# Performance work log

Measured on AMD Instinct MI355X. Metric: run time of the kernel, lower is better.

Reference implementation:

```python
import jax, jax.numpy as jnp
import numpy as np

B, S, D, H = 4, 2048, 512, 8
E = D // H  # d_head = 64

def setup_inputs() -> dict:
    key = jax.random.key(0)
    ks = jax.random.split(key, 10)
    s_in = (1.0 / np.sqrt(D))
    x  = jax.random.normal(ks[0], (B, S, D), dtype=jnp.float32)
    Wq = jax.random.normal(ks[1], (H, D, E), dtype=jnp.float32) * s_in
    bq = jax.random.normal(ks[2], (H, E), dtype=jnp.float32) * 0.01
    Wk = jax.random.normal(ks[3], (H, D, E), dtype=jnp.float32) * s_in
    bk = jax.random.normal(ks[4], (H, E), dtype=jnp.float32) * 0.01
    Wv = jax.random.normal(ks[5], (H, D, E), dtype=jnp.float32) * s_in
    bv = jax.random.normal(ks[6], (H, E), dtype=jnp.float32) * 0.01
    Wo = jax.random.normal(ks[7], (D, D), dtype=jnp.float32) * s_in
    bo = jax.random.normal(ks[8], (D,), dtype=jnp.float32) * 0.01
    return {"x": x, "Wq": Wq, "bq": bq, "Wk": Wk, "bk": bk,
            "Wv": Wv, "bv": bv, "Wo": Wo, "bo": bo}

def reference(x, Wq, bq, Wk, bk, Wv, bv, Wo, bo):
    B_, S_, D_ = x.shape
    # per-head projections (batched over head axis h)
    q = jnp.einsum('bsd,hde->bhse', x, Wq) + bq[None, :, None, :]
    k = jnp.einsum('bsd,hde->bhse', x, Wk) + bk[None, :, None, :]
    v = jnp.einsum('bsd,hde->bhse', x, Wv) + bv[None, :, None, :]
    # NOTE: original scales by d_model**-0.5 (full D), not d_head**-0.5
    scale = jnp.asarray(D_, x.dtype) ** -0.5
    scores = jnp.einsum('bhse,bhte->bhst', q, k) * scale  # [B,H,S,S]
    causal = jnp.tril(jnp.ones((S_, S_), dtype=bool))
    scores = jnp.where(causal[None, None], scores, -jnp.inf)
    attn = jax.nn.softmax(scores, axis=-1)
    out = jnp.einsum('bhst,bhte->bhse', attn, v)  # [B,H,S,E]
    # concat heads along feature dim (head-major), matching torch.cat
    out = out.transpose(0, 2, 1, 3).reshape(B_, S_, D_)
    return out @ Wo + bo  # final projection; dropout never applied in source
```

## Files before the change

### kernel.cpp

```cpp
#include <hip/hip_runtime.h>

typedef unsigned short u16;
typedef __bf16 bf16x8 __attribute__((ext_vector_type(8)));
typedef short s16x4 __attribute__((ext_vector_type(4)));
typedef short s16x8 __attribute__((ext_vector_type(8)));
typedef float f32x4 __attribute__((ext_vector_type(4)));

#define BB 4
#define SS 2048
#define DD 512
#define HH 8
#define EE 64
#define MM 8192
#define BHSE (BB*HH*SS*EE)

#define GLOBAL_AS __attribute__((address_space(1)))
#define LDS_AS    __attribute__((address_space(3)))

#define WAITV(N)    asm volatile("s_waitcnt vmcnt(" #N ")" ::: "memory")
#define WAITLGKM0() asm volatile("s_waitcnt lgkmcnt(0)" ::: "memory")
#define SBAR0()     __builtin_amdgcn_sched_barrier(0)

__device__ __forceinline__ float b2f(u16 u) {
    return __uint_as_float(((unsigned int)u) << 16);
}
__device__ __forceinline__ u16 f2b(float f) {
    unsigned int v = __float_as_uint(f);
    v += 0x7fffu + ((v >> 16) & 1u);
    return (u16)(v >> 16);
}
__device__ __forceinline__ float loadE(const void* p, size_t idx, int isbf16) {
    return isbf16 ? b2f(((const u16*)p)[idx]) : ((const float*)p)[idx];
}
__device__ __forceinline__ void load_lds16(const u16* g, u16* l) {
    __builtin_amdgcn_global_load_lds((GLOBAL_AS void*)g, (LDS_AS void*)l, 16, 0, 0);
}

__device__ __forceinline__ int detect_bf16_wave(const u16* x) {
    const int lane = threadIdx.x & 63;
    float a0 = fabsf(b2f(x[2 * lane]));
    float a1 = fabsf(b2f(x[2 * (lane + 64)]));
    int c0 = (a0 == 0.f) || (a0 > 1e-4f && a0 < 100.f);
    int c1 = (a1 == 0.f) || (a1 > 1e-4f && a1 < 100.f);
    int cnt = __popcll(__ballot(c0)) + __popcll(__ballot(c1));
    return cnt >= 96;
}

__global__ __launch_bounds__(256) void prep(
    const void* __restrict__ X,
    const void* __restrict__ Wq, const void* __restrict__ Wk,
    const void* __restrict__ Wv, const void* __restrict__ Wo,
    u16* __restrict__ Xb, u16* __restrict__ WT, u16* __restrict__ WoT,
    int* __restrict__ flag)
{
    const int isbf16 = detect_bf16_wave((const u16*)X);
    const int bid = blockIdx.x;
    const int tid = threadIdx.x;
    if (bid < 1024) {
        if (bid == 0 && tid == 0) *flag = isbf16;
        const size_t i0 = ((size_t)bid * 256 + tid) * 16;
        if (isbf16) {
            const uint4* src = (const uint4*)(((const u16*)X) + i0);
            uint4* dst = (uint4*)(Xb + i0);
            dst[0] = src[0];
            dst[1] = src[1];
        } else {
            const float* xf = ((const float*)X) + i0;
            float4 f0 = *(const float4*)xf;
            float4 f1 = *(const float4*)(xf + 4);
            float4 f2 = *(const float4*)(xf + 8);
            float4 f3 = *(const float4*)(xf + 12);
            u16 tmp[16] = { f2b(f0.x), f2b(f0.y), f2b(f0.z), f2b(f0.w),
                            f2b(f1.x), f2b(f1.y), f2b(f1.z), f2b(f1.w),
                            f2b(f2.x), f2b(f2.y), f2b(f2.z), f2b(f2.w),
                            f2b(f3.x), f2b(f3.y), f2b(f3.z), f2b(f3.w) };
            *(uint4*)(Xb + i0) = *(const uint4*)tmp;
            *(uint4*)(Xb + i0 + 8) = *(const uint4*)(tmp + 8);
        }
        return;
    }
    const int j = bid - 1024;
    const int job = j >> 6;
    const int t = j & 63;
    const void* src; u16* dst; int src_ld;
    if (job < 3) {
        const void* W = (job == 0) ? Wq : ((job == 1) ? Wk : Wv);
        int h = t >> 3, kt = t & 7;
        size_t off = (size_t)h * DD * EE + (size_t)kt * 64 * EE;
        src = isbf16 ? (const void*)(((const u16*)W) + off)
                     : (const void*)(((const float*)W) + off);
        src_ld = EE;
        dst = WT + (size_t)job * 512 * 512 + (size_t)(h * 64) * 512 + kt * 64;
    } else {
        int a = t >> 3, b = t & 7;
        size_t off = (size_t)(a * 64) * 512 + b * 64;
        src = isbf16 ? (const void*)(((const u16*)Wo) + off)
                     : (const void*)(((const float*)Wo) + off);
        src_ld = 512;
        dst = WoT + (size_t)(b * 64) * 512 + a * 64;
    }
    __shared__ __align__(16) u16 Ts[64 * 72];
#pragma unroll
    for (int it = 0; it < 2; ++it) {
        int idx = it * 256 + tid;
        int r = idx >> 3, c = (idx & 7) << 3;
        u16 tmp[8];
        if (isbf16) {
            *(bf16x8*)tmp = *(const bf16x8*)(((const u16*)src) + (size_t)r * src_ld + c);
        } else {
            const float* sp = ((const float*)src) + (size_t)r * src_ld + c;
            float4 f0 = *(const float4*)sp;
            float4 f1 = *(const float4*)(sp + 4);
            tmp[0] = f2b(f0.x); tmp[1] = f2b(f0.y); tmp[2] = f2b(f0.z); tmp[3] = f2b(f0.w);
            tmp[4] = f2b(f1.x); tmp[5] = f2b(f1.y); tmp[6] = f2b(f1.z); tmp[7] = f2b(f1.w);
        }
#pragma unroll
        for (int k = 0; k < 8; ++k) Ts[(c + k) * 72 + r] = tmp[k];
    }
    __syncthreads();
#pragma unroll
    for (int it = 0; it < 2; ++it) {
        int idx = it * 256 + tid;
        int r = idx >> 3, c = (idx & 7) << 3;
        *(bf16x8*)(dst + (size_t)r * 512 + c) = *(const bf16x8*)&Ts[r * 72 + c];
    }
}

template<int MT, int NT>
__device__ __forceinline__ void mfma_step(const u16* As, const u16* Bs,
    int mh, int nh, int lq, int quad, f32x4 acc[MT][NT])
{
    const int sw = lq & 7;
#pragma unroll
    for (int kw = 0; kw < 2; ++kw) {
        const int G = kw * 4 + quad;
        const int col = ((G ^ sw) << 3);
        bf16x8 a[MT], b[NT];
#pragma unroll
        for (int mt = 0; mt < MT; ++mt)
            a[mt] = *(const bf16x8*)&As[(mh + mt * 16 + lq) * 64 + col];
#pragma unroll
        for (int nt = 0; nt < NT; ++nt)
            b[nt] = *(const bf16x8*)&Bs[(nh + nt * 16 + lq) * 64 + col];
#pragma unroll
        for (int mt = 0; mt < MT; ++mt)
#pragma unroll
            for (int nt = 0; nt < NT; ++nt)
                acc[mt][nt] = __builtin_amdgcn_mfma_f32_16x16x32_bf16(a[mt], b[nt], acc[mt][nt], 0, 0, 0);
    }
}

__global__ __launch_bounds__(256) void gemm_qkv(
    const u16* __restrict__ Xb, const u16* __restrict__ WT,
    const void* __restrict__ bq, const void* __restrict__ bk,
    const void* __restrict__ bv, u16* __restrict__ qkv,
    const int* __restrict__ flag)
{
    const float SCALE = 0.04419417382415922f;
    const int isbf16 = *flag;
    const int l = blockIdx.x;
    const int m0 = ((l & 7) * 8 + ((l >> 3) & 7)) * 128;
    const int n0 = (l >> 6) * 128;
    const int tid = threadIdx.x;
    const int wave = tid >> 6, lane = tid & 63;
    const int lq = lane & 15, quad = lane >> 4;
    const int mh = (wave & 1) * 64, nh = (wave >> 1) * 64;
    __shared__ __align__(16) u16 As[128 * 64];
    __shared__ __align__(16) u16 Bs[128 * 64];
    f32x4 acc[4][4] = {};

    const int swz = (lane & 7) ^ ((lane >> 3) & 7);
    const size_t lane_off = (size_t)(lane >> 3) * 512 + 8 * swz;

    for (int k0 = 0; k0 < 512; k0 += 64) {
        __syncthreads();
#pragma unroll
        for (int jj = 0; jj < 4; ++jj) {
            const int c = wave * 4 + jj;
            load_lds16(Xb + (size_t)(m0 + 8 * c) * 512 + k0 + lane_off, &As[c * 512]);
            load_lds16(WT + (size_t)(n0 + 8 * c) * 512 + k0 + lane_off, &Bs[c * 512]);
        }
        __syncthreads();
        mfma_step<4, 4>(As, Bs, mh, nh, lq, quad, acc);
    }

    const int proj = n0 >> 9;
    const void* bias = (proj == 0) ? bq : ((proj == 1) ? bk : bv);
#pragma unroll
    for (int mt = 0; mt < 4; ++mt) {
#pragma unroll
        for (int nt = 0; nt < 4; ++nt) {
#pragma unroll
            for (int r = 0; r < 4; ++r) {
                int m = m0 + mh + mt * 16 + quad * 4 + r;
                int n = n0 + nh + nt * 16 + lq;
                int nn = n & 511;
                float v = acc[mt][nt][r] + loadE(bias, nn, isbf16);
                if (proj == 0) v *= SCALE;
                int b_ = m >> 11, s = m & 2047, h = nn >> 6, e = nn & 63;
                qkv[(size_t)proj * BHSE + (((size_t)(b_ * HH + h) * SS + s) * EE + e)] = f2b(v);
            }
        }
    }
}

struct VStage { uint4 va, vb; };

__device__ __forceinline__ void stageK_dma(const u16* Kh, int t0, u16* Ksb, int tid) {
    const int wave = tid >> 6, lane = tid & 63;
    const int r = lane >> 3, s = lane & 7;
#pragma unroll
    for (int jj = 0; jj < 2; ++jj) {
        const int c = wave * 2 + jj;
        const u16* g = Kh + (size_t)(t0 + 8 * c + r) * 64 + ((s ^ (r & 7)) << 3);
        load_lds16(g, Ksb + c * 512);
    }
}
__device__ __forceinline__ void stageV_load(VStage& st, const u16* Vh, int t0, int tid) {
    int t2 = 2 * (tid & 31), e8 = (tid >> 5) * 8;
    st.va = *(const uint4*)(Vh + (size_t)(t0 + t2) * 64 + e8);
    st.vb = *(const uint4*)(Vh + (size_t)(t0 + t2 + 1) * 64 + e8);
}
__device__ __forceinline__ void stageV_write(const VStage& st, u16* VTsb, int tid) {
    int t2 = 2 * (tid & 31), e8 = (tid >> 5) * 8;
    int g2 = ((t2 >> 2) & 3) * 16 + ((t2 >> 4) << 2) + (t2 & 3);
    const unsigned* pa = (const unsigned*)&st.va;
    const unsigned* pb = (const unsigned*)&st.vb;
#pragma unroll
    for (int k = 0; k < 4; ++k) {
        unsigned lo = __builtin_amdgcn_perm(pb[k], pa[k], 0x05040100u);
        unsigned hi = __builtin_amdgcn_perm(pb[k], pa[k], 0x07060302u);
        *(unsigned*)(VTsb + (e8 + 2 * k) * 72 + g2) = lo;
        *(unsigned*)(VTsb + (e8 + 2 * k + 1) * 72 + g2) = hi;
    }
}

__device__ __forceinline__ void attn_tile2(const u16* Ksb, const u16* VTsb,
    const bf16x8* qf0, const bf16x8* qf1, int lq, int quad, int qh, int th,
    bool diag, f32x4 Ot[4][2], f32x4* lfrag)
{
    const int p0 = (quad ^ (lq & 7)) << 3;
    f32x4 sc[2][2];
#pragma unroll
    for (int tj = 0; tj < 2; ++tj) {
        const u16* Krow = Ksb + ((th * 2 + tj) * 16 + lq) * 64;
        bf16x8 k0 = *(const bf16x8*)(Krow + p0);
        bf16x8 k1 = *(const bf16x8*)(Krow + (p0 ^ 32));
        __builtin_amdgcn_s_setprio(1);
#pragma unroll
        for (int f = 0; f < 2; ++f) {
            f32x4 s = {};
            s = __builtin_amdgcn_mfma_f32_16x16x32_bf16(k0, qf0[f], s, 0, 0, 0);
            s = __builtin_amdgcn_mfma_f32_16x16x32_bf16(k1, qf1[f], s, 0, 0, 0);
            sc[f][tj] = s;
        }
        __builtin_amdgcn_s_setprio(0);
    }
    union { unsigned u[4]; bf16x8 v; } ones;
    ones.u[0] = ones.u[1] = ones.u[2] = ones.u[3] = 0x3F803F80u;
    bf16x8 pf[2];
#pragma unroll
    for (int f = 0; f < 2; ++f) {
        unsigned pu[8];
#pragma unroll
        for (int tj = 0; tj < 2; ++tj)
#pragma unroll
            for (int r = 0; r < 4; ++r) {
                float p = __expf(sc[f][tj][r]);
                if (diag) {
                    int tl = (th * 2 + tj) * 16 + quad * 4 + r;
                    int ql = qh * 32 + f * 16 + lq;
                    p = (tl <= ql) ? p : 0.f;
                }
                pu[tj * 4 + r] = __float_as_uint(p);
            }
        union { unsigned u[4]; bf16x8 v; } w;
        w.u[0] = __builtin_amdgcn_perm(pu[1], pu[0], 0x07060302u);
        w.u[1] = __builtin_amdgcn_perm(pu[3], pu[2], 0x07060302u);
        w.u[2] = __builtin_amdgcn_perm(pu[5], pu[4], 0x07060302u);
        w.u[3] = __builtin_amdgcn_perm(pu[7], pu[6], 0x07060302u);
        pf[f] = w.v;
        lfrag[f] = __builtin_amdgcn_mfma_f32_16x16x32_bf16(ones.v, w.v, lfrag[f], 0, 0, 0);
    }
    __builtin_amdgcn_s_setprio(1);
#pragma unroll
    for (int et = 0; et < 4; ++et) {
        bf16x8 vf = *(const bf16x8*)(VTsb + (et * 16 + lq) * 72 + quad * 16 + th * 8);
#pragma unroll
        for (int f = 0; f < 2; ++f)
            Ot[et][f] = __builtin_amdgcn_mfma_f32_16x16x32_bf16(vf, pf[f], Ot[et][f], 0, 0, 0);
    }
    __builtin_amdgcn_s_setprio(0);
}

#define ATTN_ITER(i, CUR, STOLD, STNEW)                                        \
  {                                                                            \
    const bool m1 = ((i) + 1 <= nIt), m2 = ((i) + 2 <= nIt);                   \
    if (m1) stageK_dma(Kh, (tFirst + (i) + 1) * 64, Ks[(CUR) ^ 1], tid);       \
    SBAR0();                                                                   \
    if (m2) stageV_load(STNEW, Vh, (tFirst + (i) + 2) * 64, tid);              \
    SBAR0();                                                                   \
    attn_tile2(Ks[CUR], VTs, qf0, qf1, lq, quad, qh, th,                       \
               diagHere && ((i) == nIt), Ot, lfrag);                           \
    __builtin_amdgcn_s_barrier();        \
    SBAR0();                                                                   \
    if (m1) {                                                                  \
      if (m2) { WAITV(4); } else { WAITV(2); }                                 \
      stageV_write(STOLD, VTs, tid);                                           \
      if (m2) { WAITV(2); } else { WAITV(0); }                                 \
      WAITLGKM0();                                                             \
      __builtin_amdgcn_s_barrier();                                            \
      SBAR0();                                                                 \
    }                                                                          \
  }

__global__ __launch_bounds__(256, 4) void attn_kernel(
    const u16* __restrict__ Qg, const u16* __restrict__ Kg,
    const u16* __restrict__ Vg, u16* __restrict__ Og,
    float* __restrict__ Opart, float* __restrict__ Lpart)
{
    const int bh = blockIdx.x;
    const int j  = (int)gridDim.y - 1 - (int)blockIdx.y;
    const int c  = blockIdx.z;
    if (c && j < 16) return;
    const int qb = j * 64;
    const int tFirst = c * 16;
    const int tLast  = (j < tFirst + 15) ? j : (tFirst + 15);
    const int nIt = tLast - tFirst;
    const bool diagHere = (tLast == j);
    const bool partial = (j >= 16);

    const int tid = threadIdx.x;
    const int wave = tid >> 6, lane = tid & 63;
    const int lq = lane & 15, quad = lane >> 4;
    const int qh = wave & 1, th = wave >> 1;
    const int b = bh >> 3, h = bh & 7;

    const size_t base = (size_t)bh * SS * EE;
    const u16* Kh = Kg + base;
    const u16* Vh = Vg + base;

    __shared__ __align__(16) u16 Ks[2][64 * 64];
    __shared__ __align__(16) u16 VTs[64 * 72];

    bf16x8 qf0[2], qf1[2];
#pragma unroll
    for (int f = 0; f < 2; ++f) {
        const int qrow_f = qb + qh * 32 + f * 16 + lq;
        const u16* Qp = Qg + base + (size_t)qrow_f * EE;
        qf0[f] = *(const bf16x8*)(Qp + quad * 8);
        qf1[f] = *(const bf16x8*)(Qp + 32 + quad * 8);
    }

    f32x4 Ot[4][2] = {};
    f32x4 lfrag[2] = {};
    VStage stA, stB;

    stageK_dma(Kh, tFirst * 64, Ks[0], tid);
    SBAR0();
    stageV_load(stA, Vh, tFirst * 64, tid);
    SBAR0();
    if (nIt >= 1) {
        stageV_load(stB, Vh, (tFirst + 1) * 64, tid);
        SBAR0();
        WAITV(2);
    } else {
        WAITV(0);
    }
    stageV_write(stA, VTs, tid);
    WAITLGKM0();
    __builtin_amdgcn_s_barrier();
    SBAR0();

    for (int i = 0; ; i += 2) {
        ATTN_ITER(i, 0, stB, stA);
        if (i + 1 > nIt) break;
        ATTN_ITER(i + 1, 1, stA, stB);
        if (i + 2 > nIt) break;
    }

    __syncthreads();
    float* redO = (float*)&Ks[0][0];
    float* redL = (float*)&VTs[0];
    if (th == 1) {
#pragma unroll
        for (int et = 0; et < 4; ++et)
#pragma unroll
            for (int f = 0; f < 2; ++f)
                *(f32x4*)&redO[(((qh * 4 + et) * 2 + f) * 64 + lane) * 4] = Ot[et][f];
#pragma unroll
        for (int f = 0; f < 2; ++f)
            redL[(qh * 2 + f) * 64 + lane] = lfrag[f][0];
    }
    __syncthreads();
    if (th == 1) return;
    float lf[2];
#pragma unroll
    for (int f = 0; f < 2; ++f)
        lf[f] = lfrag[f][0] + redL[(qh * 2 + f) * 64 + lane];
#pragma unroll
    for (int et = 0; et < 4; ++et)
#pragma unroll
        for (int f = 0; f < 2; ++f)
            Ot[et][f] += *(const f32x4*)&redO[(((qh * 4 + et) * 2 + f) * 64 + lane) * 4];

    if (!partial) {
#pragma unroll
        for (int f = 0; f < 2; ++f) {
            const float inv = 1.f / lf[f];
            const int qrow_f = qb + qh * 32 + f * 16 + lq;
            u16* Op = Og + (((size_t)(b * SS + qrow_f)) * HH + h) * EE;
#pragma unroll
            for (int et = 0; et < 4; ++et) {
                u16 tmp[4];
#pragma unroll
                for (int r = 0; r < 4; ++r) tmp[r] = f2b(Ot[et][f][r] * inv);
                *(uint2*)(Op + et * 16 + quad * 4) = *(const uint2*)tmp;
            }
        }
    } else {
        const size_t slot = ((size_t)(bh * 16 + (j - 16)) * 2 + c);
        float* Os = Opart + slot * 4096;
#pragma unroll
        for (int f = 0; f < 2; ++f) {
            const int ql = qh * 32 + f * 16 + lq;
#pragma unroll
            for (int et = 0; et < 4; ++et)
                *(f32x4*)&Os[ql * 64 + et * 16 + quad * 4] = Ot[et][f];
            if (quad == 0) Lpart[slot * 64 + ql] = lf[f];
        }
    }
}

__global__ __launch_bounds__(256) void attn_merge(
    const float* __restrict__ Opart, const float* __restrict__ Lpart,
    u16* __restrict__ Og)
{
    const int tg = blockIdx.x * 256 + threadIdx.x;
    const int e8 = (tg & 7) * 8;
    const int rest = tg >> 3;
    const int bh = rest >> 10;
    const int sp = rest & 1023;
    const int jj = sp >> 6;
    const int ql = sp & 63;
    const size_t slot = (size_t)(bh * 16 + jj) * 2;
    const size_t o0 = slot * 4096 + (size_t)ql * 64 + e8;
    float4 a0 = *(const float4*)&Opart[o0];
    float4 a1 = *(const float4*)&Opart[o0 + 4];
    float4 b0 = *(const float4*)&Opart[o0 + 4096];
    float4 b1 = *(const float4*)&Opart[o0 + 4096 + 4];
    const size_t ls = slot * 64 + ql;
    const float inv = 1.f / (Lpart[ls] + Lpart[ls + 64]);
    const int b = bh >> 3, h = bh & 7;
    const int s = 1024 + sp;
    u16 tmp[8];
    tmp[0] = f2b((a0.x + b0.x) * inv);
    tmp[1] = f2b((a0.y + b0.y) * inv);
    tmp[2] = f2b((a0.z + b0.z) * inv);
    tmp[3] = f2b((a0.w + b0.w) * inv);
    tmp[4] = f2b((a1.x + b1.x) * inv);
    tmp[5] = f2b((a1.y + b1.y) * inv);
    tmp[6] = f2b((a1.z + b1.z) * inv);
    tmp[7] = f2b((a1.w + b1.w) * inv);
    u16* Op = Og + (((size_t)(b * SS + s)) * HH + h) * EE + e8;
    *(uint4*)Op = *(const uint4*)tmp;
}

__global__ __launch_bounds__(256) void gemm_out(
    const u16* __restrict__ A, const u16* __restrict__ WoT,
    const void* __restrict__ bo, void* __restrict__ out,
    const int* __restrict__ flag)
{
    const int isbf16 = *flag;
    const int l = blockIdx.x;
    const int m0 = ((l & 7) * 8 + ((l >> 3) & 7)) * 128;
    const int n0 = (l >> 6) * 64;
    const int tid = threadIdx.x;
    const int wave = tid >> 6, lane = tid & 63;
    const int lq = lane & 15, quad = lane >> 4;
    const int mh = (wave & 1) * 64, nh = (wave >> 1) * 32;
    __shared__ __align__(16) u16 As[128 * 64];
    __shared__ __align__(16) u16 Bs[64 * 64];
    f32x4 acc[4][2] = {};

    const int swz = (lane & 7) ^ ((lane >> 3) & 7);
    const size_t lane_off = (size_t)(lane >> 3) * 512 + 8 * swz;

    for (int k0 = 0; k0 < 512; k0 += 64) {
        __syncthreads();
#pragma unroll
        for (int jj = 0; jj < 4; ++jj) {
            const int c = wave * 4 + jj;
            load_lds16(A + (size_t)(m0 + 8 * c) * 512 + k0 + lane_off, &As[c * 512]);
        }
#pragma unroll
        for (int jj = 0; jj < 2; ++jj) {
            const int c = wave * 2 + jj;
            load_lds16(WoT + (size_t)(n0 + 8 * c) * 512 + k0 + lane_off, &Bs[c * 512]);
        }
        __syncthreads();
        mfma_step<4, 2>(As, Bs, mh, nh, lq, quad, acc);
    }
#pragma unroll
    for (int mt = 0; mt < 4; ++mt) {
#pragma unroll
        for (int nt = 0; nt < 2; ++nt) {
#pragma unroll
            for (int r = 0; r < 4; ++r) {
                int m = m0 + mh + mt * 16 + quad * 4 + r;
                int n = n0 + nh + nt * 16 + lq;
                float v = acc[mt][nt][r] + loadE(bo, n, isbf16);
                if (isbf16) ((u16*)out)[(size_t)m * 512 + n] = f2b(v);
                else        ((float*)out)[(size_t)m * 512 + n] = v;
            }
        }
    }
}

extern "C" void kernel_launch(void* const* d_in, const int* in_sizes, int n_in,
                              void* d_out, int out_size, void* d_ws, size_t ws_size,
                              hipStream_t stream) {
    const void* x  = d_in[0];
    const void* Wq = d_in[1];
    const void* bq = d_in[2];
    const void* Wk = d_in[3];
    const void* bk = d_in[4];
    const void* Wv = d_in[5];
    const void* bv = d_in[6];
    const void* Wo = d_in[7];
    const void* bo = d_in[8];

    u16* WT   = (u16*)d_ws;
    u16* WoT  = WT + 3 * 512 * 512;
    u16* qkv  = WoT + 512 * 512;
    u16* attn = qkv + 3 * (size_t)BHSE;
    int* flag = (int*)(attn + (size_t)BHSE);
    u16* Xb   = (u16*)(flag + 8);
    float* Opart = (float*)(Xb + (size_t)MM * DD);
    float* Lpart = Opart + (size_t)1024 * 4096;

    prep<<<1024 + 256, 256, 0, stream>>>(x, Wq, Wk, Wv, Wo, Xb, WT, WoT, flag);
    gemm_qkv<<<(MM / 128) * (1536 / 128), 256, 0, stream>>>(Xb, WT, bq, bk, bv, qkv, flag);
    attn_kernel<<<dim3(BB * HH, SS / 64, 2), 256, 0, stream>>>(
        qkv, qkv + BHSE, qkv + 2 * (size_t)BHSE, attn, Opart, Lpart);
    attn_merge<<<1024, 256, 0, stream>>>(Opart, Lpart, attn);
    gemm_out<<<(MM / 128) * (512 / 64), 256, 0, stream>>>(attn, WoT, bo, d_out, flag);
}
```

Baseline: 174.1 us.

## Fuse split-KV merge into attention kernel via atomic last-block reduction

Removes the separate attn_merge kernel. Each split block that handles a partial query tile writes its partial O and L, then increments an atomic counter per slot. The second block to arrive reads the other block's partial and writes the normalized bf16 output. Counters are zeroed in the prep kernel. This saves one kernel launch and its extra pass over memory. In exchange it adds threadfences, an atomic, and extra barriers in the attention epilogue.

```diff
diff --git a/kernel.cpp b/kernel.cpp
--- a/kernel.cpp
+++ b/kernel.cpp
@@ -51,13 +51,17 @@
     const void* __restrict__ Wq, const void* __restrict__ Wk,
     const void* __restrict__ Wv, const void* __restrict__ Wo,
     u16* __restrict__ Xb, u16* __restrict__ WT, u16* __restrict__ WoT,
-    int* __restrict__ flag)
+    int* __restrict__ flag, int* __restrict__ cnt)
 {
     const int isbf16 = detect_bf16_wave((const u16*)X);
     const int bid = blockIdx.x;
     const int tid = threadIdx.x;
     if (bid < 1024) {
-        if (bid == 0 && tid == 0) *flag = isbf16;
+        if (bid == 0) {
+            if (tid == 0) *flag = isbf16;
+            cnt[tid] = 0;
+            cnt[tid + 256] = 0;
+        }
         const size_t i0 = ((size_t)bid * 256 + tid) * 16;
         if (isbf16) {
             const uint4* src = (const uint4*)(((const u16*)X) + i0);
@@ -317,7 +321,8 @@
 __global__ __launch_bounds__(256, 4) void attn_kernel(
     const u16* __restrict__ Qg, const u16* __restrict__ Kg,
     const u16* __restrict__ Vg, u16* __restrict__ Og,
-    float* __restrict__ Opart, float* __restrict__ Lpart)
+    float* __restrict__ Opart, float* __restrict__ Lpart,
+    int* __restrict__ cnt)
 {
     const int bh = blockIdx.x;
     const int j  = (int)gridDim.y - 1 - (int)blockIdx.y;
@@ -393,18 +398,57 @@
             redL[(qh * 2 + f) * 64 + lane] = lfrag[f][0];
     }
     __syncthreads();
-    if (th == 1) return;
-    float lf[2];
-#pragma unroll
-    for (int f = 0; f < 2; ++f)
-        lf[f] = lfrag[f][0] + redL[(qh * 2 + f) * 64 + lane];
-#pragma unroll
-    for (int et = 0; et < 4; ++et)
+    float lf[2] = {0.f, 0.f};
+    if (th == 0) {
 #pragma unroll
         for (int f = 0; f < 2; ++f)
-            Ot[et][f] += *(const f32x4*)&redO[(((qh * 4 + et) * 2 + f) * 64 + lane) * 4];
-
-    if (!partial) {
+            lf[f] = lfrag[f][0] + redL[(qh * 2 + f) * 64 + lane];
+#pragma unroll
+        for (int et = 0; et < 4; ++et)
+#pragma unroll
+            for (int f = 0; f < 2; ++f)
+                Ot[et][f] += *(const f32x4*)&redO[(((qh * 4 + et) * 2 + f) * 64 + lane) * 4];
+    }
+
+    if (partial) {
+        const int pslot = bh * 16 + (j - 16);
+        const size_t slot = (size_t)pslot * 2 + c;
+        if (th == 0) {
+            float* Os = Opart + slot * 4096;
+#pragma unroll
+            for (int f = 0; f < 2; ++f) {
+                const int ql = qh * 32 + f * 16 + lq;
+#pragma unroll
+                for (int et = 0; et < 4; ++et)
+                    *(f32x4*)&Os[ql * 64 + et * 16 + quad * 4] = Ot[et][f];
+                if (quad == 0) Lpart[slot * 64 + ql] = lf[f];
+            }
+        }
+        __syncthreads();
+        volatile int* tick = (volatile int*)((int*)&VTs[0] + 512);
+        if (tid == 0) {
+            __threadfence();
+            tick[0] = atomicAdd(&cnt[pslot], 1);
+        }
+        __syncthreads();
+        if (tick[0] == 0) return;
+        if (th == 1) return;
+        __threadfence();
+        const size_t oslot = (size_t)pslot * 2 + (c ^ 1);
+        const float* Oo = Opart + oslot * 4096;
+#pragma unroll
+        for (int f = 0; f < 2; ++f) {
+            const int ql = qh * 32 + f * 16 + lq;
+            lf[f] += Lpart[oslot * 64 + ql];
+#pragma unroll
+            for (int et = 0; et < 4; ++et)
+                Ot[et][f] += *(const f32x4*)&Oo[ql * 64 + et * 16 + quad * 4];
+        }
+    } else if (th == 1) {
+        return;
+    }
+
+    if (th == 0) {
 #pragma unroll
         for (int f = 0; f < 2; ++f) {
             const float inv = 1.f / lf[f];
@@ -418,52 +462,7 @@
                 *(uint2*)(Op + et * 16 + quad * 4) = *(const uint2*)tmp;
             }
         }
-    } else {
-        const size_t slot = ((size_t)(bh * 16 + (j - 16)) * 2 + c);
-        float* Os = Opart + slot * 4096;
-#pragma unroll
-        for (int f = 0; f < 2; ++f) {
-            const int ql = qh * 32 + f * 16 + lq;
-#pragma unroll
-            for (int et = 0; et < 4; ++et)
-                *(f32x4*)&Os[ql * 64 + et * 16 + quad * 4] = Ot[et][f];
-            if (quad == 0) Lpart[slot * 64 + ql] = lf[f];
-        }
-    }
-}
-
-__global__ __launch_bounds__(256) void attn_merge(
-    const float* __restrict__ Opart, const float* __restrict__ Lpart,
-    u16* __restrict__ Og)
-{
-    const int tg = blockIdx.x * 256 + threadIdx.x;
-    const int e8 = (tg & 7) * 8;
-    const int rest = tg >> 3;
-    const int bh = rest >> 10;
-    const int sp = rest & 1023;
-    const int jj = sp >> 6;
-    const int ql = sp & 63;
-    const size_t slot = (size_t)(bh * 16 + jj) * 2;
-    const size_t o0 = slot * 4096 + (size_t)ql * 64 + e8;
-    float4 a0 = *(const float4*)&Opart[o0];
-    float4 a1 = *(const float4*)&Opart[o0 + 4];
-    float4 b0 = *(const float4*)&Opart[o0 + 4096];
-    float4 b1 = *(const float4*)&Opart[o0 + 4096 + 4];
-    const size_t ls = slot * 64 + ql;
-    const float inv = 1.f / (Lpart[ls] + Lpart[ls + 64]);
-    const int b = bh >> 3, h = bh & 7;
-    const int s = 1024 + sp;
-    u16 tmp[8];
-    tmp[0] = f2b((a0.x + b0.x) * inv);
-    tmp[1] = f2b((a0.y + b0.y) * inv);
-    tmp[2] = f2b((a0.z + b0.z) * inv);
-    tmp[3] = f2b((a0.w + b0.w) * inv);
-    tmp[4] = f2b((a1.x + b1.x) * inv);
-    tmp[5] = f2b((a1.y + b1.y) * inv);
-    tmp[6] = f2b((a1.z + b1.z) * inv);
-    tmp[7] = f2b((a1.w + b1.w) * inv);
-    u16* Op = Og + (((size_t)(b * SS + s)) * HH + h) * EE + e8;
-    *(uint4*)Op = *(const uint4*)tmp;
+    }
 }
 
 __global__ __launch_bounds__(256) void gemm_out(
@@ -538,11 +537,11 @@
     u16* Xb   = (u16*)(flag + 8);
     float* Opart = (float*)(Xb + (size_t)MM * DD);
     float* Lpart = Opart + (size_t)1024 * 4096;
-
-    prep<<<1024 + 256, 256, 0, stream>>>(x, Wq, Wk, Wv, Wo, Xb, WT, WoT, flag);
+    int*   cnt   = (int*)(Lpart + (size_t)1024 * 64);
+
+    prep<<<1024 + 256, 256, 0, stream>>>(x, Wq, Wk, Wv, Wo, Xb, WT, WoT, flag, cnt);
     gemm_qkv<<<(MM / 128) * (1536 / 128), 256, 0, stream>>>(Xb, WT, bq, bk, bv, qkv, flag);
     attn_kernel<<<dim3(BB * HH, SS / 64, 2), 256, 0, stream>>>(
-        qkv, qkv + BHSE, qkv + 2 * (size_t)BHSE, attn, Opart, Lpart);
-    attn_merge<<<1024, 256, 0, stream>>>(Opart, Lpart, attn);
+        qkv, qkv + BHSE, qkv + 2 * (size_t)BHSE, attn, Opart, Lpart, cnt);
     gemm_out<<<(MM / 128) * (512 / 64), 256, 0, stream>>>(attn, WoT, bo, d_out, flag);
 }
```

Result: slower. 244.7 us (+40.6%).
